# Optimization experiments

Hardware: AMD Instinct MI355X
Metric: run time of the kernel (lower is better)

Reference implementation:

```python
import jax, jax.numpy as jnp
import numpy as np

HEAD = 16  # attention heads


def setup_inputs() -> dict:
    key = jax.random.key(0)
    ks = jax.random.split(key, 8)
    n, c, ph = 1024, 512, 8
    N = ph * ph
    inter = c // 2
    inp = {
        "query": jax.random.normal(ks[0], (n, c, ph, ph), jnp.float32),
        "context": jax.random.normal(ks[1], (n, c, ph, ph), jnp.float32),
        "Wm": jax.random.normal(ks[2], (HEAD, N, N), jnp.float32) * 0.02,
        "bm": jnp.zeros((HEAD, N), jnp.float32),
        "Wg": jax.random.normal(ks[3], (inter, c), jnp.float32) * 0.02,
        "bg": jnp.zeros((inter,), jnp.float32),
        "Wt": jax.random.normal(ks[4], (inter, c), jnp.float32) * 0.02,
        "bt": jnp.zeros((inter,), jnp.float32),
        "Wp": jax.random.normal(ks[5], (inter, c), jnp.float32) * 0.02,
        "bp": jnp.zeros((inter,), jnp.float32),
        "Wo": jax.random.normal(ks[6], (c, inter), jnp.float32) * 0.02,
        "bo": jnp.zeros((c,), jnp.float32),
    }
    return inp


def reference(query, context, Wm, bm, Wg, bg, Wt, bt, Wp, bp, Wo, bo):
    n, c, h, w = query.shape
    N = h * w
    inter = Wg.shape[0]
    dh = inter // HEAD  # per-head dim

    # --- position mixing (per-head Linear over the N token dim) ---
    ctx = context.reshape(n, c, N)
    ctx_r = ctx.reshape(n, HEAD, c // HEAD, N)
    mixed = jnp.einsum('nhdk,hok->nhdo', ctx_r, Wm) + bm[None, :, None, :]
    ctx = ctx + mixed.reshape(n, c, N)

    # --- 1x1 conv projections (g, theta, phi) ---
    g_x = jnp.einsum('ncx,oc->nox', ctx, Wg) + bg[None, :, None]
    phi_x = jnp.einsum('ncx,oc->nox', ctx, Wp) + bp[None, :, None]
    theta_x = jnp.einsum('ncx,oc->nox', query.reshape(n, c, N), Wt) + bt[None, :, None]

    g_x = g_x.reshape(n, HEAD, dh, N)
    phi_x = phi_x.reshape(n, HEAD, dh, N)
    theta_x = theta_x.reshape(n, HEAD, dh, N)

    # --- embedded_gaussian attention with scaling ---
    scores = jnp.einsum('nhdq,nhdk->nhqk', theta_x, phi_x) / jnp.sqrt(jnp.float32(dh))
    w_attn = jax.nn.softmax(scores, axis=-1)
    y = jnp.einsum('nhqk,nhdk->nhdq', w_attn, g_x).reshape(n, inter, N)

    # --- conv_out (1x1) + residual ---
    out_y = jnp.einsum('ncx,oc->nox', y, Wo) + bo[None, :, None]
    return query + out_y.reshape(n, c, h, w)
```

## Files before the change

kernel.cpp:

```cpp
#include <hip/hip_runtime.h>
#include <hip/hip_bf16.h>

using u16 = unsigned short;
using u32 = unsigned int;
typedef __attribute__((ext_vector_type(8))) short short8;
typedef __attribute__((ext_vector_type(4))) float f32x4;

__device__ __forceinline__ float bf2f(u16 x){ return __uint_as_float(((u32)x)<<16); }
__device__ __forceinline__ u16 f2bf(float f){
  u32 u = __float_as_uint(f);
  u += 0x7fffu + ((u>>16)&1u);
  return (u16)(u>>16);
}
__device__ __forceinline__ u32 cvtpk(float a, float b){
  u32 r;
  asm("v_cvt_pk_bf16_f32 %0, %1, %2" : "=v"(r) : "v"(a), "v"(b));
  return r;
}
__device__ __forceinline__ short8 pack8(float4 a, float4 b){
  union { short8 s; u32 u[4]; } r;
  r.u[0] = (u32)f2bf(a.x) | ((u32)f2bf(a.y)<<16);
  r.u[1] = (u32)f2bf(a.z) | ((u32)f2bf(a.w)<<16);
  r.u[2] = (u32)f2bf(b.x) | ((u32)f2bf(b.y)<<16);
  r.u[3] = (u32)f2bf(b.z) | ((u32)f2bf(b.w)<<16);
  return r.s;
}
#define MFMA(a,b,c) __builtin_amdgcn_mfma_f32_16x16x32_bf16((a),(b),(c),0,0,0)


__global__ __launch_bounds__(256) void k_prep(
    const float* __restrict__ Wt, const float* __restrict__ Wp,
    const float* __restrict__ Wg, const float* __restrict__ Wo,
    const float* __restrict__ Wm, u16* __restrict__ wb)
{
  int i8 = (blockIdx.x*256 + threadIdx.x)*8;
  const float* src; int local;
  if      (i8 < 131072){ src = Wt; local = i8; }
  else if (i8 < 262144){ src = Wp; local = i8-131072; }
  else if (i8 < 393216){ src = Wg; local = i8-262144; }
  else if (i8 < 524288){ src = Wo; local = i8-393216; }
  else                 { src = Wm; local = i8-524288; }
  float4 a = *(const float4*)(src+local);
  float4 b = *(const float4*)(src+local+4);
  union { short8 s; uint4 u; } r;
  r.s = pack8(a,b);
  *(uint4*)(wb + i8) = r.u;
}

__global__ __launch_bounds__(256) void k_posmix(
    const float* __restrict__ ctx, const u16* __restrict__ wm_b,
    const float* __restrict__ bm, u16* __restrict__ ctxp)
{
  int lane = threadIdx.x & 63;
  int l15 = lane & 15, q = lane >> 4;
  int wv = (blockIdx.x<<2) + (threadIdx.x>>6);
  int n = wv >> 4, h = wv & 15;
  const float* cbase = ctx + (size_t)n*32768 + h*2048;
  const u16*  wmb   = wm_b + h*4096;
  const f32x4 Z = {0.f,0.f,0.f,0.f};
  f32x4 acc[2][4];
  #pragma unroll
  for (int mi=0;mi<2;mi++)
    #pragma unroll
    for (int ni=0;ni<4;ni++) acc[mi][ni] = Z;

  #pragma unroll
  for (int ks=0; ks<2; ks++){
    short8 a[2], b[4];
    #pragma unroll
    for (int mi=0; mi<2; mi++){
      const float* ap = cbase + (mi*16 + l15)*64 + ks*32 + q*8;
      float4 v0 = *(const float4*)ap;
      float4 v1 = *(const float4*)(ap+4);
      a[mi] = pack8(v0, v1);
    }
    #pragma unroll
    for (int ni=0; ni<4; ni++)
      b[ni] = *(const short8*)(wmb + (ni*16 + l15)*64 + ks*32 + q*8);
    #pragma unroll
    for (int mi=0;mi<2;mi++)
      #pragma unroll
      for (int ni=0;ni<4;ni++) acc[mi][ni] = MFMA(a[mi], b[ni], acc[mi][ni]);
  }

  float bmv[4];
  #pragma unroll
  for (int ni=0;ni<4;ni++) bmv[ni] = bm[h*64 + ni*16 + l15];
  u16* obase = ctxp + (size_t)n*32768 + h*2048;
  #pragma unroll
  for (int mi=0;mi<2;mi++)
    #pragma unroll
    for (int r=0;r<4;r++){
      int row = mi*16 + q*4 + r;
      #pragma unroll
      for (int ni=0;ni<4;ni++){
        int col = ni*16 + l15;
        float res = cbase[row*64 + col];
        obase[row*64 + col] = f2bf(acc[mi][ni][r] + bmv[ni] + res);
      }
    }
}

__global__ __launch_bounds__(256) void k_proj(
    const float* __restrict__ query, const u16* __restrict__ ctxp,
    const u16* __restrict__ wb, const float* __restrict__ bt,
    const float* __restrict__ bp, const float* __restrict__ bg,
    u16* __restrict__ theta, u16* __restrict__ phi, u16* __restrict__ g)
{
  __shared__ __align__(16) u16 sb[64*44 + 16];
  int t = threadIdx.x;
  int lane = t & 63, l15 = lane & 15, q = lane >> 4, w = t >> 6;
  int n = blockIdx.x, tensor = blockIdx.y;
  const u16* W = wb + tensor*131072;
  const float* bias = (tensor==0) ? bt : (tensor==1) ? bp : bg;
  u16* dst = (tensor==0) ? theta : (tensor==1) ? phi : g;
  bool sw = (tensor < 2);

  const f32x4 Z = {0.f,0.f,0.f,0.f};
  f32x4 acc[4][4];
  #pragma unroll
  for (int mi=0;mi<4;mi++)
    #pragma unroll
    for (int ni=0;ni<4;ni++) acc[mi][ni] = Z;

  int sc = (t>>4)*2;
  int sx = (t&15)*4;

  for (int ks=0; ks<16; ks++){
    int k0 = ks*32;
    if (tensor == 0){
      const float* s0 = query + (size_t)n*32768 + (size_t)(k0+sc)*64 + sx;
      float4 va = *(const float4*)s0;
      float4 vb = *(const float4*)(s0 + 64);
      *(u32*)&sb[(sx+0)*44 + sc] = (u32)f2bf(va.x) | ((u32)f2bf(vb.x)<<16);
      *(u32*)&sb[(sx+1)*44 + sc] = (u32)f2bf(va.y) | ((u32)f2bf(vb.y)<<16);
      *(u32*)&sb[(sx+2)*44 + sc] = (u32)f2bf(va.z) | ((u32)f2bf(vb.z)<<16);
      *(u32*)&sb[(sx+3)*44 + sc] = (u32)f2bf(va.w) | ((u32)f2bf(vb.w)<<16);
    } else {
      const u16* s0 = ctxp + (size_t)n*32768 + (size_t)(k0+sc)*64 + sx;
      uint2 ua = *(const uint2*)s0;
      uint2 ub = *(const uint2*)(s0 + 64);
      *(u32*)&sb[(sx+0)*44 + sc] = (ua.x & 0xffffu) | ((ub.x & 0xffffu)<<16);
      *(u32*)&sb[(sx+1)*44 + sc] = (ua.x >> 16)     | (ub.x & 0xffff0000u);
      *(u32*)&sb[(sx+2)*44 + sc] = (ua.y & 0xffffu) | ((ub.y & 0xffffu)<<16);
      *(u32*)&sb[(sx+3)*44 + sc] = (ua.y >> 16)     | (ub.y & 0xffff0000u);
    }
    __syncthreads();
    short8 wf[4], sf[4];
    #pragma unroll
    for (int mi=0;mi<4;mi++)
      wf[mi] = *(const short8*)(W + (size_t)(w*64 + mi*16 + l15)*512 + k0 + q*8);
    #pragma unroll
    for (int ni=0;ni<4;ni++){
      union { short8 s; uint2 u[2]; } bb;
      int bidx = (ni*16 + l15)*44 + q*8;
      bb.u[0] = *(const uint2*)&sb[bidx];
      bb.u[1] = *(const uint2*)&sb[bidx + 4];
      sf[ni] = bb.s;
    }
    if (sw){
      #pragma unroll
      for (int mi=0;mi<4;mi++)
        #pragma unroll
        for (int ni=0;ni<4;ni++) acc[mi][ni] = MFMA(sf[mi], wf[ni], acc[mi][ni]);
    } else {
      #pragma unroll
      for (int mi=0;mi<4;mi++)
        #pragma unroll
        for (int ni=0;ni<4;ni++) acc[mi][ni] = MFMA(wf[mi], sf[ni], acc[mi][ni]);
    }
    __syncthreads();
  }

  if (!sw){
    u16* dbase = dst + (size_t)n*16384;
    #pragma unroll
    for (int mi=0;mi<4;mi++)
      #pragma unroll
      for (int r=0;r<4;r++){
        int row = w*64 + mi*16 + q*4 + r;
        float bv = bias[row];
        #pragma unroll
        for (int ni=0;ni<4;ni++){
          int col = ni*16 + l15;
          dbase[row*64 + col] = f2bf(acc[mi][ni][r] + bv);
        }
      }
  } else {
    u16* dbase = dst + (size_t)n*16384 + (size_t)w*4096;
    float bv[4];
    #pragma unroll
    for (int j=0;j<4;j++) bv[j] = bias[w*64 + j*16 + l15];
    #pragma unroll
    for (int i=0;i<4;i++)
      #pragma unroll
      for (int r=0;r<4;r++){
        int x = i*16 + q*4 + r;
        #pragma unroll
        for (int j=0;j<4;j++)
          dbase[j*1024 + x*16 + l15] = f2bf(acc[i][j][r] + bv[j]);
      }
  }
}

__global__ __launch_bounds__(256) void k_attn(
    const u16* __restrict__ thetaT, const u16* __restrict__ phiT,
    const u16* __restrict__ g, u16* __restrict__ yT)
{
  __shared__ __align__(16) u16 pbuf[4][4096];
  int lane = threadIdx.x & 63;
  int w = threadIdx.x >> 6;
  int wv = (blockIdx.x<<2) + w;
  int n = wv >> 4, h = wv & 15;
  int l15 = lane & 15, grp = lane >> 4;

  const u16* thB = thetaT + (size_t)n*16384 + h*1024;
  const u16* phB = phiT   + (size_t)n*16384 + h*1024;
  const u16* gB  = g      + (size_t)n*16384 + h*1024;

  const f32x4 Z = {0.f,0.f,0.f,0.f};

  short8 zz; { union{ short8 s; u32 u[4]; } z; z.u[0]=z.u[1]=z.u[2]=z.u[3]=0; zz=z.s; }
  bool real = grp < 2;
  short8 aF[4], bF[4];
  #pragma unroll
  for (int kt=0;kt<4;kt++)
    aF[kt] = real ? *(const short8*)(phB + (kt*16+l15)*16 + grp*8) : zz;
  #pragma unroll
  for (int qt=0;qt<4;qt++)
    bF[qt] = real ? *(const short8*)(thB + (qt*16+l15)*16 + grp*8) : zz;

  f32x4 s[4][4];
  #pragma unroll
  for (int qt=0;qt<4;qt++)
    #pragma unroll
    for (int kt=0;kt<4;kt++)
      s[qt][kt] = MFMA(aF[kt], bF[qt], Z);

  char* pl = (char*)pbuf[w];
  float inv[4];
  #pragma unroll
  for (int qt=0;qt<4;qt++){
    float m = s[qt][0][0];
    #pragma unroll
    for (int kt=0;kt<4;kt++)
      m = fmaxf(m, fmaxf(fmaxf(s[qt][kt][0], s[qt][kt][1]),
                         fmaxf(s[qt][kt][2], s[qt][kt][3])));
    m = fmaxf(m, __shfl_xor(m, 16));
    m = fmaxf(m, __shfl_xor(m, 32));
    float sum = 0.f;
    #pragma unroll
    for (int kt=0;kt<4;kt++)
      #pragma unroll
      for (int r=0;r<4;r++){
        float p = __expf((s[qt][kt][r] - m)*0.25f);
        s[qt][kt][r] = p;
        sum += p;
      }
    sum += __shfl_xor(sum, 16);
    sum += __shfl_xor(sum, 32);
    inv[qt] = 1.f / sum;
    int qq = qt*16 + l15;
    int swz = (qq & 7) << 4;
    #pragma unroll
    for (int kt=0;kt<4;kt++){
      u32 lo = cvtpk(s[qt][kt][0], s[qt][kt][1]);
      u32 hi = cvtpk(s[qt][kt][2], s[qt][kt][3]);
      *(uint2*)(pl + qq*128 + ((kt*32 + grp*8) ^ swz)) = make_uint2(lo, hi);
    }
  }

  short8 ga[2];
  #pragma unroll
  for (int ks=0;ks<2;ks++)
    ga[ks] = *(const short8*)(gB + l15*64 + ks*32 + grp*8);

  u16* yb = yT + (size_t)n*16384 + (size_t)h*16 + grp*4;
  #pragma unroll
  for (int Q=0;Q<4;Q++){
    int qq = Q*16 + l15;
    int swz = (qq & 7) << 4;
    f32x4 acc = Z;
    #pragma unroll
    for (int ks=0;ks<2;ks++){
      short8 pb = *(const short8*)(pl + qq*128 + ((ks*64 + grp*16) ^ swz));
      acc = MFMA(ga[ks], pb, acc);
    }
    float iv = inv[Q];
    u32 o0 = cvtpk(acc[0]*iv, acc[1]*iv);
    u32 o1 = cvtpk(acc[2]*iv, acc[3]*iv);
    *(uint2*)(yb + (size_t)qq*256) = make_uint2(o0, o1);
  }
}

__global__ __launch_bounds__(256) void k_out(
    const float* __restrict__ query, const u16* __restrict__ yT,
    const u16* __restrict__ wo_b, const float* __restrict__ bo,
    float* __restrict__ out)
{
  int t = threadIdx.x, lane = t & 63, l15 = lane & 15, q = lane >> 4, w = t >> 6;
  int n = blockIdx.x;
  int mbase = blockIdx.y*256 + w*64;
  const f32x4 Z = {0.f,0.f,0.f,0.f};
  f32x4 acc[4][4];
  #pragma unroll
  for (int mi=0;mi<4;mi++)
    #pragma unroll
    for (int ni=0;ni<4;ni++) acc[mi][ni] = Z;

  #pragma unroll 2
  for (int ks=0; ks<8; ks++){
    int k0 = ks*32;
    short8 a[4], b[4];
    #pragma unroll
    for (int mi=0;mi<4;mi++)
      a[mi] = *(const short8*)(wo_b + (size_t)(mbase + mi*16 + l15)*256 + k0 + q*8);
    #pragma unroll
    for (int ni=0;ni<4;ni++)
      b[ni] = *(const short8*)(yT + (size_t)n*16384 + (size_t)(ni*16 + l15)*256 + k0 + q*8);
    #pragma unroll
    for (int mi=0;mi<4;mi++)
      #pragma unroll
      for (int ni=0;ni<4;ni++) acc[mi][ni] = MFMA(a[mi], b[ni], acc[mi][ni]);
  }

  #pragma unroll
  for (int mi=0;mi<4;mi++)
    #pragma unroll
    for (int r=0;r<4;r++){
      int row = mbase + mi*16 + q*4 + r;
      float bv = bo[row];
      #pragma unroll
      for (int ni=0;ni<4;ni++){
        int col = ni*16 + l15;
        size_t idx = (size_t)n*32768 + (size_t)row*64 + col;
        out[idx] = acc[mi][ni][r] + bv + query[idx];
      }
    }
}

extern "C" void kernel_launch(void* const* d_in, const int* in_sizes, int n_in,
                              void* d_out, int out_size, void* d_ws, size_t ws_size,
                              hipStream_t stream)
{
  const float* query = (const float*)d_in[0];
  const float* ctx   = (const float*)d_in[1];
  const float* Wm    = (const float*)d_in[2];
  const float* bm    = (const float*)d_in[3];
  const float* Wg    = (const float*)d_in[4];
  const float* bg    = (const float*)d_in[5];
  const float* Wt    = (const float*)d_in[6];
  const float* bt    = (const float*)d_in[7];
  const float* Wp    = (const float*)d_in[8];
  const float* bp    = (const float*)d_in[9];
  const float* Wo    = (const float*)d_in[10];
  const float* bo    = (const float*)d_in[11];

  u16* wb    = (u16*)d_ws;
  u16* ctxp  = wb + 589824;
  u16* theta = ctxp + 33554432;
  u16* phi   = theta + 16777216;
  u16* g     = phi + 16777216;
  u16* yTb   = ctxp;
  float* outp = (float*)d_out;

  hipLaunchKernelGGL(k_prep,   dim3(288),     dim3(256), 0, stream, Wt,Wp,Wg,Wo,Wm, wb);
  hipLaunchKernelGGL(k_posmix, dim3(4096),    dim3(256), 0, stream, ctx, wb+524288, bm, ctxp);
  hipLaunchKernelGGL(k_proj,   dim3(1024,3),  dim3(256), 0, stream,
                     query, ctxp, wb, bt, bp, bg, theta, phi, g);
  hipLaunchKernelGGL(k_attn,   dim3(4096),    dim3(256), 0, stream, theta, phi, g, yTb);
  hipLaunchKernelGGL(k_out,    dim3(1024,2),  dim3(256), 0, stream, query, yTb, wb+393216, bo, outp);
}
```

Before: 606.1 us.

## Double-buffer LDS tiles and prefetch next K-slice in projection kernel

The k_proj loop now uses two shared-memory buffers and issues the global loads for the next 32-wide K slice (activations and weight fragments) before running the current slice's MFMAs. The prefetched data is written to the alternate buffer afterwards, which drops one barrier per iteration. The intent is to hide global memory latency behind the matrix math. In exchange it doubles the LDS footprint and adds registers for the prefetched values, which may lower occupancy.

Measured after the change: 581.3 us. 1.04x faster.

```diff
diff --git a/kernel.cpp b/kernel.cpp
--- a/kernel.cpp
+++ b/kernel.cpp
@@ -107,7 +107,7 @@
     const float* __restrict__ bp, const float* __restrict__ bg,
     u16* __restrict__ theta, u16* __restrict__ phi, u16* __restrict__ g)
 {
-  __shared__ __align__(16) u16 sb[64*44 + 16];
+  __shared__ __align__(16) u16 sb[2][64*44 + 16];
   int t = threadIdx.x;
   int lane = t & 63, l15 = lane & 15, q = lane >> 4, w = t >> 6;
   int n = blockIdx.x, tensor = blockIdx.y;
@@ -126,36 +126,66 @@
   int sc = (t>>4)*2;
   int sx = (t&15)*4;
 
+  const float* qsrc = query + (size_t)n*32768 + (size_t)sc*64 + sx;
+  const u16*  csrc = ctxp  + (size_t)n*32768 + (size_t)sc*64 + sx;
+
+  {
+    u16* sbn = sb[0];
+    if (tensor == 0){
+      float4 va = *(const float4*)qsrc;
+      float4 vb = *(const float4*)(qsrc + 64);
+      *(u32*)&sbn[(sx+0)*44 + sc] = (u32)f2bf(va.x) | ((u32)f2bf(vb.x)<<16);
+      *(u32*)&sbn[(sx+1)*44 + sc] = (u32)f2bf(va.y) | ((u32)f2bf(vb.y)<<16);
+      *(u32*)&sbn[(sx+2)*44 + sc] = (u32)f2bf(va.z) | ((u32)f2bf(vb.z)<<16);
+      *(u32*)&sbn[(sx+3)*44 + sc] = (u32)f2bf(va.w) | ((u32)f2bf(vb.w)<<16);
+    } else {
+      uint2 ua = *(const uint2*)csrc;
+      uint2 ub = *(const uint2*)(csrc + 64);
+      *(u32*)&sbn[(sx+0)*44 + sc] = (ua.x & 0xffffu) | ((ub.x & 0xffffu)<<16);
+      *(u32*)&sbn[(sx+1)*44 + sc] = (ua.x >> 16)     | (ub.x & 0xffff0000u);
+      *(u32*)&sbn[(sx+2)*44 + sc] = (ua.y & 0xffffu) | ((ub.y & 0xffffu)<<16);
+      *(u32*)&sbn[(sx+3)*44 + sc] = (ua.y >> 16)     | (ub.y & 0xffff0000u);
+    }
+  }
+  short8 wf[4];
+  #pragma unroll
+  for (int mi=0;mi<4;mi++)
+    wf[mi] = *(const short8*)(W + (size_t)(w*64 + mi*16 + l15)*512 + q*8);
+  __syncthreads();
+
+  #pragma unroll 2
   for (int ks=0; ks<16; ks++){
+    const u16* sbc = sb[ks&1];
+    u16* sbn = sb[(ks+1)&1];
     int k0 = ks*32;
-    if (tensor == 0){
-      const float* s0 = query + (size_t)n*32768 + (size_t)(k0+sc)*64 + sx;
-      float4 va = *(const float4*)s0;
-      float4 vb = *(const float4*)(s0 + 64);
-      *(u32*)&sb[(sx+0)*44 + sc] = (u32)f2bf(va.x) | ((u32)f2bf(vb.x)<<16);
-      *(u32*)&sb[(sx+1)*44 + sc] = (u32)f2bf(va.y) | ((u32)f2bf(vb.y)<<16);
-      *(u32*)&sb[(sx+2)*44 + sc] = (u32)f2bf(va.z) | ((u32)f2bf(vb.z)<<16);
-      *(u32*)&sb[(sx+3)*44 + sc] = (u32)f2bf(va.w) | ((u32)f2bf(vb.w)<<16);
-    } else {
-      const u16* s0 = ctxp + (size_t)n*32768 + (size_t)(k0+sc)*64 + sx;
-      uint2 ua = *(const uint2*)s0;
-      uint2 ub = *(const uint2*)(s0 + 64);
-      *(u32*)&sb[(sx+0)*44 + sc] = (ua.x & 0xffffu) | ((ub.x & 0xffffu)<<16);
-      *(u32*)&sb[(sx+1)*44 + sc] = (ua.x >> 16)     | (ub.x & 0xffff0000u);
-      *(u32*)&sb[(sx+2)*44 + sc] = (ua.y & 0xffffu) | ((ub.y & 0xffffu)<<16);
-      *(u32*)&sb[(sx+3)*44 + sc] = (ua.y >> 16)     | (ub.y & 0xffff0000u);
-    }
-    __syncthreads();
-    short8 wf[4], sf[4];
-    #pragma unroll
-    for (int mi=0;mi<4;mi++)
-      wf[mi] = *(const short8*)(W + (size_t)(w*64 + mi*16 + l15)*512 + k0 + q*8);
+    bool more = (ks < 15);
+
+    float4 pva, pvb; uint2 pua, pub;
+    if (more){
+      if (tensor == 0){
+        const float* s0 = qsrc + (size_t)(k0+32)*64;
+        pva = *(const float4*)s0;
+        pvb = *(const float4*)(s0 + 64);
+      } else {
+        const u16* s0 = csrc + (size_t)(k0+32)*64;
+        pua = *(const uint2*)s0;
+        pub = *(const uint2*)(s0 + 64);
+      }
+    }
+    short8 wn[4];
+    if (more){
+      #pragma unroll
+      for (int mi=0;mi<4;mi++)
+        wn[mi] = *(const short8*)(W + (size_t)(w*64 + mi*16 + l15)*512 + k0+32 + q*8);
+    }
+
+    short8 sf[4];
     #pragma unroll
     for (int ni=0;ni<4;ni++){
       union { short8 s; uint2 u[2]; } bb;
       int bidx = (ni*16 + l15)*44 + q*8;
-      bb.u[0] = *(const uint2*)&sb[bidx];
-      bb.u[1] = *(const uint2*)&sb[bidx + 4];
+      bb.u[0] = *(const uint2*)&sbc[bidx];
+      bb.u[1] = *(const uint2*)&sbc[bidx + 4];
       sf[ni] = bb.s;
     }
     if (sw){
@@ -169,7 +199,23 @@
         #pragma unroll
         for (int ni=0;ni<4;ni++) acc[mi][ni] = MFMA(wf[mi], sf[ni], acc[mi][ni]);
     }
-    __syncthreads();
+
+    if (more){
+      if (tensor == 0){
+        *(u32*)&sbn[(sx+0)*44 + sc] = (u32)f2bf(pva.x) | ((u32)f2bf(pvb.x)<<16);
+        *(u32*)&sbn[(sx+1)*44 + sc] = (u32)f2bf(pva.y) | ((u32)f2bf(pvb.y)<<16);
+        *(u32*)&sbn[(sx+2)*44 + sc] = (u32)f2bf(pva.z) | ((u32)f2bf(pvb.z)<<16);
+        *(u32*)&sbn[(sx+3)*44 + sc] = (u32)f2bf(pva.w) | ((u32)f2bf(pvb.w)<<16);
+      } else {
+        *(u32*)&sbn[(sx+0)*44 + sc] = (pua.x & 0xffffu) | ((pub.x & 0xffffu)<<16);
+        *(u32*)&sbn[(sx+1)*44 + sc] = (pua.x >> 16)     | (pub.x & 0xffff0000u);
+        *(u32*)&sbn[(sx+2)*44 + sc] = (pua.y & 0xffffu) | ((pub.y & 0xffffu)<<16);
+        *(u32*)&sbn[(sx+3)*44 + sc] = (pua.y >> 16)     | (pub.y & 0xffff0000u);
+      }
+      __syncthreads();
+      #pragma unroll
+      for (int mi=0;mi<4;mi++) wf[mi] = wn[mi];
+    }
   }
 
   if (!sw){
```
